# Kernel optimization log

Measured on AMD Instinct MI355X. Metric: run time of the kernel, lower is better.

The kernel has to match this reference:

```python
import jax, jax.numpy as jnp
import numpy as np

B, T, H, NH = 16, 2048, 1024, 16
HD = H // NH  # 64
IN0, IN1 = 256, 512  # modality input sizes needing projection; modality 2 is already H


def _ln(x, g, b, eps=1e-5):
    m = jnp.mean(x, axis=-1, keepdims=True)
    v = jnp.mean((x - m) ** 2, axis=-1, keepdims=True)
    return (x - m) / jnp.sqrt(v + eps) * g + b


def setup_inputs() -> dict:
    key = jax.random.key(0)
    ks = jax.random.split(key, 24)
    s = 0.02
    d = {
        'x0': jax.random.normal(ks[0], (B, T, IN0), jnp.float32),
        'x1': jax.random.normal(ks[1], (B, T, IN1), jnp.float32),
        'x2': jax.random.normal(ks[2], (B, T, H), jnp.float32),
        'static_context': jax.random.normal(ks[3], (B, T, H), jnp.float32),
        'Wp0': jax.random.normal(ks[4], (H, IN0), jnp.float32) * s,
        'bp0': jnp.zeros((H,), jnp.float32),
        'Wp1': jax.random.normal(ks[5], (H, IN1), jnp.float32) * s,
        'bp1': jnp.zeros((H,), jnp.float32),
        'Wq': jax.random.normal(ks[6], (H, H), jnp.float32) * s,
        'bq': jnp.zeros((H,), jnp.float32),
        'Wk': jax.random.normal(ks[7], (H, H), jnp.float32) * s,
        'bk': jnp.zeros((H,), jnp.float32),
        'Wv': jax.random.normal(ks[8], (H, H), jnp.float32) * s,
        'bv': jnp.zeros((H,), jnp.float32),
        'Wo': jax.random.normal(ks[9], (H, H), jnp.float32) * s,
        'bo': jnp.zeros((H,), jnp.float32),
        'query_token': jax.random.normal(ks[10], (H,), jnp.float32) * s,
        'g1': jnp.ones((H,), jnp.float32),
        'be1': jnp.zeros((H,), jnp.float32),
        'g2': jnp.ones((H,), jnp.float32),
        'be2': jnp.zeros((H,), jnp.float32),
        'W1': jax.random.normal(ks[11], (4 * H, H), jnp.float32) * s,
        'b1': jnp.zeros((4 * H,), jnp.float32),
        'W2': jax.random.normal(ks[12], (H, 4 * H), jnp.float32) * s,
        'b2': jnp.zeros((H,), jnp.float32),
    }
    return d


def _forward(x0, x1, x2, static_context, Wp0, bp0, Wp1, bp1, Wq, bq, Wk, bk, Wv, bv,
             Wo, bo, query_token, g1, be1, g2, be2, W1, b1, W2, b2):
    # project modalities to hidden size, stack -> [B, T, M, H]
    m0 = x0 @ Wp0.T + bp0
    m1 = x1 @ Wp1.T + bp1
    stacked = jnp.stack([m0, m1, x2], axis=2)  # [B,T,3,H]
    M = stacked.shape[2]
    # per-timestep single-query cross-attention over the M modality tokens,
    # batched over all B*T positions (equivalent to the torch per-t loop)
    q = query_token + static_context  # [B,T,H]
    Q = (q @ Wq.T + bq).reshape(B, T, NH, HD)
    K = (stacked @ Wk.T + bk).reshape(B, T, M, NH, HD)
    V = (stacked @ Wv.T + bv).reshape(B, T, M, NH, HD)
    scores = jnp.einsum('bthd,btmhd->bthm', Q, K) / jnp.sqrt(jnp.asarray(HD, Q.dtype))
    attn = jax.nn.softmax(scores, axis=-1)  # [B,T,NH,M]
    weights = attn.mean(axis=2)  # average over heads (torch default) -> [B,T,M]
    ctx = jnp.einsum('bthm,btmhd->bthd', attn, V).reshape(B, T, H)
    attn_out = ctx @ Wo.T + bo
    fused = _ln(attn_out, g1, be1)
    ff = jax.nn.gelu(fused @ W1.T + b1, approximate=False) @ W2.T + b2
    fused = _ln(fused + ff, g2, be2)
    return fused, weights


def reference(x0, x1, x2, static_context, Wp0, bp0, Wp1, bp1, Wq, bq, Wk, bk, Wv, bv,
              Wo, bo, query_token, g1, be1, g2, be2, W1, b1, W2, b2):
    return _forward(x0, x1, x2, static_context, Wp0, bp0, Wp1, bp1, Wq, bq, Wk, bk,
                    Wv, bv, Wo, bo, query_token, g1, be1, g2, be2, W1, b1, W2, b2)
```

## Files before the change

kernel.cpp:

```cpp
#include <hip/hip_runtime.h>
#include <hip/hip_bf16.h>
#include <math.h>

#define BT 32768
#define HH 1024

typedef unsigned short u16;
typedef __attribute__((ext_vector_type(4))) unsigned short u16x4;
typedef __attribute__((ext_vector_type(8))) __bf16 bf16x8;
typedef __attribute__((ext_vector_type(4))) float f32x4;

#define DEVI static __device__ __forceinline__

DEVI u16 f2bf(float f){
  unsigned u = __builtin_bit_cast(unsigned, f);
  u += 0x7FFFu + ((u >> 16) & 1u);
  return (u16)(u >> 16);
}
DEVI float bf2f(u16 h){
  unsigned u = ((unsigned)h) << 16;
  return __builtin_bit_cast(float, u);
}
DEVI void gl_lds16(const void* g, void* l){
  __builtin_amdgcn_global_load_lds((const __attribute__((address_space(1))) void*)g,
                                   (__attribute__((address_space(3))) void*)l, 16, 0, 0);
}
DEVI int swz(int row, int elem){ return elem ^ ((row & 7) << 3); }

__global__ void k_cast4(const float* __restrict__ s, u16* __restrict__ d, int n4){
  int i = blockIdx.x*blockDim.x + threadIdx.x;
  int st = gridDim.x*blockDim.x;
  for (; i < n4; i += st){
    float4 v = ((const float4*)s)[i];
    u16x4 o = { f2bf(v.x), f2bf(v.y), f2bf(v.z), f2bf(v.w) };
    ((u16x4*)d)[i] = o;
  }
}

__global__ void k_qb(const float* __restrict__ qt, const float* __restrict__ sc,
                     u16* __restrict__ d, int n4){
  int i = blockIdx.x*blockDim.x + threadIdx.x;
  int st = gridDim.x*blockDim.x;
  for (; i < n4; i += st){
    int e = i*4; int c = e & 1023;
    float4 v = *(const float4*)&sc[e];
    float4 q = *(const float4*)&qt[c];
    u16x4 o = { f2bf(v.x+q.x), f2bf(v.y+q.y), f2bf(v.z+q.z), f2bf(v.w+q.w) };
    ((u16x4*)d)[i] = o;
  }
}

__global__ void k_copyf(const float* __restrict__ s, float* __restrict__ d, int n){
  int i = blockIdx.x*blockDim.x + threadIdx.x;
  int st = gridDim.x*blockDim.x;
  for (; i < n; i += st) d[i] = s[i];
}

__global__ void k_transcast(const float* __restrict__ s, u16* __restrict__ d, int R, int C){
  __shared__ float tile[32][33];
  int c0 = blockIdx.x*32, r0 = blockIdx.y*32;
  int tx = threadIdx.x & 31, ty = threadIdx.x >> 5;
  #pragma unroll
  for (int i = 0; i < 32; i += 8) tile[ty+i][tx] = s[(size_t)(r0+ty+i)*C + c0+tx];
  __syncthreads();
  #pragma unroll
  for (int i = 0; i < 32; i += 8) d[(size_t)(c0+ty+i)*R + r0+tx] = f2bf(tile[tx][ty+i]);
}

__global__ void k_matvec(const u16* __restrict__ W, const float* __restrict__ x,
                         const float* __restrict__ badd, float* __restrict__ out, int K){
  int row = blockIdx.x*4 + (threadIdx.x>>6);
  int lane = threadIdx.x & 63;
  float s = 0.f;
  for (int k = lane; k < K; k += 64) s += bf2f(W[(size_t)row*K + k]) * x[k];
  #pragma unroll
  for (int m = 1; m < 64; m <<= 1) s += __shfl_xor(s, m);
  if (lane == 0) out[row] = s + badd[row];
}

__global__ __launch_bounds__(256, 3)
void k_gemm(const u16* __restrict__ A, int lda,
            const u16* __restrict__ B, int ldb, int K,
            const float* __restrict__ bias,
            u16* __restrict__ C, int ldc, int col0, int act)
{
  __shared__ u16 As[128*64];
  __shared__ u16 Bs[128*64];
  const int tid = threadIdx.x, lane = tid & 63, wid = tid >> 6;
  const int wr = wid >> 1, wc = wid & 1;
  const int r15 = lane & 15, g = lane >> 4;
  const int m0 = blockIdx.x * 128, n0 = blockIdx.y * 128;
  f32x4 acc[4][4] = {};

  for (int k0 = 0; k0 < K; k0 += 64){
    #pragma unroll
    for (int it = 0; it < 4; ++it){
      int c = it*256 + tid;
      int row = c >> 3;
      int ke = swz(row, (c & 7) * 8);
      gl_lds16(A + (size_t)(m0+row)*lda + (k0+ke), As + c*8);
      gl_lds16(B + (size_t)(n0+row)*ldb + (k0+ke), Bs + c*8);
    }
    __syncthreads();
    #pragma unroll
    for (int kk = 0; kk < 64; kk += 32){
      bf16x8 av[4], bvv[4];
      #pragma unroll
      for (int i = 0; i < 4; ++i){
        int row = wr*64 + i*16 + r15;
        av[i] = *(const bf16x8*)&As[row*64 + swz(row, kk + g*8)];
      }
      #pragma unroll
      for (int j = 0; j < 4; ++j){
        int row = wc*64 + j*16 + r15;
        bvv[j] = *(const bf16x8*)&Bs[row*64 + swz(row, kk + g*8)];
      }
      #pragma unroll
      for (int i = 0; i < 4; ++i)
        #pragma unroll
        for (int j = 0; j < 4; ++j)
          acc[i][j] = __builtin_amdgcn_mfma_f32_16x16x32_bf16(av[i], bvv[j], acc[i][j], 0, 0, 0);
    }
    __syncthreads();
  }
  #pragma unroll
  for (int j = 0; j < 4; ++j){
    int col = wc*64 + j*16 + r15;
    float bb = bias ? bias[n0 + col] : 0.f;
    #pragma unroll
    for (int i = 0; i < 4; ++i){
      #pragma unroll
      for (int jj = 0; jj < 4; ++jj){
        int row = wr*64 + i*16 + g*4 + jj;
        float v = acc[i][j][jj] + bb;
        if (act == 1) v = 0.5f * v * (1.f + erff(v * 0.70710678118654752f));
        C[(size_t)(m0+row)*ldc + col0 + n0 + col] = f2bf(v);
      }
    }
  }
}

__global__ __launch_bounds__(512, 4)
void k_attn2p(const u16* __restrict__ x0b, const u16* __restrict__ x1b, const u16* __restrict__ x2b,
              const u16* __restrict__ Wc0, const u16* __restrict__ Wc1, const u16* __restrict__ Wc2,
              const float* __restrict__ bc0, const float* __restrict__ bc1, const float* __restrict__ bc2,
              const u16* __restrict__ Qg, u16* __restrict__ ctx, float* __restrict__ wacc)
{
  __shared__ __align__(16) u16 As[128*64];
  __shared__ __align__(16) u16 Bs[128*64];
  __shared__ float Sl[2*128*3];

  const int tid = threadIdx.x, lane = tid & 63, wid = tid >> 6;
  const int wr = wid >> 1, h = wid & 1;
  const int r15 = lane & 15, g = lane >> 4;
  const int bid = blockIdx.x;
  const int bn = bid & 7, btb = bid >> 3;
  const int t0 = btb * 128, n0 = bn * 128;

  const u16* Xs[3] = { x0b, x1b, x2b };
  const u16* Ws[3] = { Wc0, Wc1, Wc2 };
  const float* Bc[3] = { bc0, bc1, bc2 };
  const int Ks[3] = { 256, 512, 1024 };

  const int srow = tid >> 3;
  const int scol = (tid & 7) * 8;

  #pragma unroll
  for (int m = 0; m < 3; ++m){
    const int K = Ks[m];
    const u16* X = Xs[m];
    const u16* W = Ws[m];
    f32x4 aK[2][4] = {};
    for (int k0 = 0; k0 < K; k0 += 64){
      #pragma unroll
      for (int l = 0; l < 2; ++l){
        int row = l*64 + srow;
        int ke = swz(row, scol);
        gl_lds16(X + (size_t)(t0+row)*K + k0 + ke, &As[row*64 + scol]);
        gl_lds16(W + (size_t)(n0+row)*K + k0 + ke, &Bs[row*64 + scol]);
      }
      __syncthreads();
      #pragma unroll
      for (int kk = 0; kk < 64; kk += 32){
        bf16x8 av[2], bv[4];
        #pragma unroll
        for (int i = 0; i < 2; ++i){
          int ra = wr*32 + i*16 + r15;
          av[i] = *(const bf16x8*)&As[ra*64 + swz(ra, kk + g*8)];
        }
        #pragma unroll
        for (int j = 0; j < 4; ++j){
          int rb = h*64 + j*16 + r15;
          bv[j] = *(const bf16x8*)&Bs[rb*64 + swz(rb, kk + g*8)];
        }
        #pragma unroll
        for (int i = 0; i < 2; ++i)
          #pragma unroll
          for (int j = 0; j < 4; ++j)
            aK[i][j] = __builtin_amdgcn_mfma_f32_16x16x32_bf16(av[i], bv[j], aK[i][j], 0, 0, 0);
      }
      __syncthreads();
    }
    float bkc[4];
    #pragma unroll
    for (int j = 0; j < 4; ++j) bkc[j] = Bc[m][n0 + h*64 + j*16 + r15];
    #pragma unroll
    for (int i = 0; i < 2; ++i){
      #pragma unroll
      for (int jj = 0; jj < 4; ++jj){
        int tt = wr*32 + i*16 + g*4 + jj;
        const u16* qrow = Qg + (size_t)(t0+tt)*1024 + n0 + h*64 + r15;
        float s = 0.f;
        #pragma unroll
        for (int j = 0; j < 4; ++j)
          s += (aK[i][j][jj] + bkc[j]) * bf2f(qrow[j*16]);
        s += __shfl_xor(s, 1); s += __shfl_xor(s, 2);
        s += __shfl_xor(s, 4); s += __shfl_xor(s, 8);
        if (r15 == 0) Sl[(h*128 + tt)*3 + m] = s * 0.125f;
      }
    }
  }
  __syncthreads();
  if (tid < 256){
    int h2 = tid >> 7, tt = tid & 127;
    int base = (h2*128 + tt)*3;
    float s0 = Sl[base+0], s1 = Sl[base+1], s2 = Sl[base+2];
    float mx = fmaxf(s0, fmaxf(s1, s2));
    float e0 = expf(s0-mx), e1 = expf(s1-mx), e2 = expf(s2-mx);
    float inv = 1.f/(e0+e1+e2);
    e0 *= inv; e1 *= inv; e2 *= inv;
    Sl[base+0] = e0; Sl[base+1] = e1; Sl[base+2] = e2;
    atomicAdd(&wacc[(size_t)(t0+tt)*3 + 0], e0*0.0625f);
    atomicAdd(&wacc[(size_t)(t0+tt)*3 + 1], e1*0.0625f);
    atomicAdd(&wacc[(size_t)(t0+tt)*3 + 2], e2*0.0625f);
  }
  __syncthreads();

  f32x4 ctxa[2][4] = {};
  #pragma unroll
  for (int m = 0; m < 3; ++m){
    const int K = Ks[m];
    const u16* X = Xs[m];
    const u16* W = Ws[m] + (size_t)1024*K;
    f32x4 aV[2][4] = {};
    for (int k0 = 0; k0 < K; k0 += 64){
      #pragma unroll
      for (int l = 0; l < 2; ++l){
        int row = l*64 + srow;
        int ke = swz(row, scol);
        gl_lds16(X + (size_t)(t0+row)*K + k0 + ke, &As[row*64 + scol]);
        gl_lds16(W + (size_t)(n0+row)*K + k0 + ke, &Bs[row*64 + scol]);
      }
      __syncthreads();
      #pragma unroll
      for (int kk = 0; kk < 64; kk += 32){
        bf16x8 av[2], bv[4];
        #pragma unroll
        for (int i = 0; i < 2; ++i){
          int ra = wr*32 + i*16 + r15;
          av[i] = *(const bf16x8*)&As[ra*64 + swz(ra, kk + g*8)];
        }
        #pragma unroll
        for (int j = 0; j < 4; ++j){
          int rb = h*64 + j*16 + r15;
          bv[j] = *(const bf16x8*)&Bs[rb*64 + swz(rb, kk + g*8)];
        }
        #pragma unroll
        for (int i = 0; i < 2; ++i)
          #pragma unroll
          for (int j = 0; j < 4; ++j)
            aV[i][j] = __builtin_amdgcn_mfma_f32_16x16x32_bf16(av[i], bv[j], aV[i][j], 0, 0, 0);
      }
      __syncthreads();
    }
    #pragma unroll
    for (int j = 0; j < 4; ++j){
      float bvv = Bc[m][1024 + n0 + h*64 + j*16 + r15];
      #pragma unroll
      for (int i = 0; i < 2; ++i){
        #pragma unroll
        for (int jj = 0; jj < 4; ++jj){
          int tt = wr*32 + i*16 + g*4 + jj;
          float p = Sl[(h*128 + tt)*3 + m];
          ctxa[i][j][jj] += p * (aV[i][j][jj] + bvv);
        }
      }
    }
  }
  #pragma unroll
  for (int i = 0; i < 2; ++i){
    #pragma unroll
    for (int jj = 0; jj < 4; ++jj){
      int tt = wr*32 + i*16 + g*4 + jj;
      #pragma unroll
      for (int j = 0; j < 4; ++j)
        ctx[(size_t)(t0+tt)*1024 + n0 + h*64 + j*16 + r15] = f2bf(ctxa[i][j][jj]);
    }
  }
}

__global__ __launch_bounds__(256)
void k_ln(const u16* __restrict__ X, const u16* __restrict__ R,
          const float* __restrict__ gam, const float* __restrict__ bet,
          u16* __restrict__ outb, float* __restrict__ outf)
{
  __shared__ float rs[4], rq[4];
  const int t = blockIdx.x, tid = threadIdx.x;
  const size_t base = (size_t)t*1024 + tid*4;
  u16x4 xv = *(const u16x4*)&X[base];
  float v[4];
  #pragma unroll
  for (int i = 0; i < 4; ++i) v[i] = bf2f(xv[i]);
  if (R){
    u16x4 rv = *(const u16x4*)&R[base];
    #pragma unroll
    for (int i = 0; i < 4; ++i) v[i] += bf2f(rv[i]);
  }
  float s = v[0]+v[1]+v[2]+v[3];
  float q = v[0]*v[0]+v[1]*v[1]+v[2]*v[2]+v[3]*v[3];
  #pragma unroll
  for (int m = 1; m < 64; m <<= 1){ s += __shfl_xor(s, m); q += __shfl_xor(q, m); }
  if ((tid & 63) == 0){ rs[tid>>6] = s; rq[tid>>6] = q; }
  __syncthreads();
  s = rs[0]+rs[1]+rs[2]+rs[3];
  q = rq[0]+rq[1]+rq[2]+rq[3];
  float mean = s * (1.f/1024.f);
  float var  = q * (1.f/1024.f) - mean*mean;
  float rstd = rsqrtf(var + 1e-5f);
  int c0 = tid*4;
  if (outb){
    u16x4 o;
    #pragma unroll
    for (int i = 0; i < 4; ++i) o[i] = f2bf((v[i]-mean)*rstd*gam[c0+i] + bet[c0+i]);
    *(u16x4*)&outb[base] = o;
  } else {
    float4 o;
    o.x = (v[0]-mean)*rstd*gam[c0+0] + bet[c0+0];
    o.y = (v[1]-mean)*rstd*gam[c0+1] + bet[c0+1];
    o.z = (v[2]-mean)*rstd*gam[c0+2] + bet[c0+2];
    o.w = (v[3]-mean)*rstd*gam[c0+3] + bet[c0+3];
    *(float4*)&outf[base] = o;
  }
}

extern "C" void kernel_launch(void* const* d_in, const int* in_sizes, int n_in,
                              void* d_out, int out_size, void* d_ws, size_t ws_size,
                              hipStream_t stream)
{
  (void)in_sizes; (void)n_in; (void)out_size;
  const float* x0  = (const float*)d_in[0];
  const float* x1  = (const float*)d_in[1];
  const float* x2  = (const float*)d_in[2];
  const float* sc  = (const float*)d_in[3];
  const float* Wp0 = (const float*)d_in[4];  const float* bp0 = (const float*)d_in[5];
  const float* Wp1 = (const float*)d_in[6];  const float* bp1 = (const float*)d_in[7];
  const float* Wq  = (const float*)d_in[8];  const float* bq  = (const float*)d_in[9];
  const float* Wk  = (const float*)d_in[10]; const float* bk  = (const float*)d_in[11];
  const float* Wv  = (const float*)d_in[12]; const float* bv  = (const float*)d_in[13];
  const float* Wo  = (const float*)d_in[14]; const float* bo  = (const float*)d_in[15];
  const float* qt  = (const float*)d_in[16];
  const float* g1  = (const float*)d_in[17]; const float* be1 = (const float*)d_in[18];
  const float* g2  = (const float*)d_in[19]; const float* be2 = (const float*)d_in[20];
  const float* W1  = (const float*)d_in[21]; const float* b1  = (const float*)d_in[22];
  const float* W2  = (const float*)d_in[23]; const float* b2  = (const float*)d_in[24];

  char* ws = (char*)d_ws;
  size_t off = 0;
  auto alloc = [&](size_t b)->char*{ char* p = ws + off; off += (b + 255) & ~(size_t)255; return p; };

  u16* Wqb   = (u16*)alloc((size_t)1024*1024*2);
  u16* Wob   = (u16*)alloc((size_t)1024*1024*2);
  u16* W1b   = (u16*)alloc((size_t)4096*1024*2);
  u16* W2b   = (u16*)alloc((size_t)1024*4096*2);
  u16* Wkvb  = (u16*)alloc((size_t)2048*1024*2);
  u16* Wp0t  = (u16*)alloc((size_t)256*1024*2);
  u16* Wp1t  = (u16*)alloc((size_t)512*1024*2);
  u16* Wkv0c = (u16*)alloc((size_t)2048*256*2);
  u16* Wkv1c = (u16*)alloc((size_t)2048*512*2);
  float* bc0 = (float*)alloc((size_t)2048*4);
  float* bc1 = (float*)alloc((size_t)2048*4);
  float* bc2 = (float*)alloc((size_t)2048*4);
  char* regX  = alloc((size_t)BT*(256+512+1024)*2);
  char* regQ1 = alloc((size_t)BT*1024*2);
  char* regQ2 = alloc((size_t)BT*1024*2);
  float* wacc = (float*)alloc((size_t)BT*3*4);
  if (off > ws_size) return;

  u16* x0b = (u16*)regX;
  u16* x1b = (u16*)(regX + (size_t)BT*256*2);
  u16* x2b = (u16*)(regX + (size_t)BT*768*2);
  u16* aob  = (u16*)regX;
  u16* ff2b = (u16*)regX;
  u16* qb   = (u16*)regQ1;
  u16* ctxb = (u16*)regQ1;
  u16* f1b  = (u16*)regQ1;
  u16* Qb   = (u16*)regQ2;
  u16* ff1c = (u16*)regQ2;

  hipMemsetAsync(wacc, 0, (size_t)BT*3*4, stream);

  dim3 B256(256), B512(512);
  auto cast4 = [&](const float* s, u16* d, int n, int grid){
    k_cast4<<<dim3(grid), B256, 0, stream>>>(s, d, n >> 2);
  };
  cast4(Wq, Wqb, 1024*1024, 1024);
  cast4(Wk, Wkvb, 1024*1024, 1024);
  cast4(Wv, Wkvb + (size_t)1024*1024, 1024*1024, 1024);
  cast4(Wo, Wob, 1024*1024, 1024);
  cast4(W1, W1b, 4096*1024, 1024);
  cast4(W2, W2b, 4096*1024, 1024);
  cast4(x0, x0b, BT*256, 1024);
  cast4(x1, x1b, BT*512, 1024);
  cast4(x2, x2b, BT*1024, 2048);
  k_transcast<<<dim3(8, 32),  B256, 0, stream>>>(Wp0, Wp0t, 1024, 256);
  k_transcast<<<dim3(16, 32), B256, 0, stream>>>(Wp1, Wp1t, 1024, 512);
  k_copyf<<<dim3(4), B256, 0, stream>>>(bk, bc2, 1024);
  k_copyf<<<dim3(4), B256, 0, stream>>>(bv, bc2 + 1024, 1024);
  k_matvec<<<dim3(512), B256, 0, stream>>>(Wkvb, bp0, bc2, bc0, 1024);
  k_matvec<<<dim3(512), B256, 0, stream>>>(Wkvb, bp1, bc2, bc1, 1024);
  k_qb<<<dim3(2048), B256, 0, stream>>>(qt, sc, qb, BT*256);

  k_gemm<<<dim3(16, 2), B256, 0, stream>>>(Wkvb, 1024, Wp0t, 1024, 1024, nullptr, Wkv0c, 256, 0, 0);
  k_gemm<<<dim3(16, 4), B256, 0, stream>>>(Wkvb, 1024, Wp1t, 1024, 1024, nullptr, Wkv1c, 512, 0, 0);

  k_gemm<<<dim3(BT/128, 8), B256, 0, stream>>>(qb, 1024, Wqb, 1024, 1024, bq, Qb, 1024, 0, 0);
  k_attn2p<<<dim3(BT/128*8), B512, 0, stream>>>(x0b, x1b, x2b, Wkv0c, Wkv1c, Wkvb,
                                                bc0, bc1, bc2, Qb, ctxb, wacc);
  k_gemm<<<dim3(BT/128, 8), B256, 0, stream>>>(ctxb, 1024, Wob, 1024, 1024, bo, aob, 1024, 0, 0);
  k_ln<<<dim3(BT), B256, 0, stream>>>(aob, nullptr, g1, be1, f1b, nullptr);

  for (int c = 0; c < 4; ++c){
    const u16* fa = f1b + (size_t)c*8192*1024;
    k_gemm<<<dim3(64, 32), B256, 0, stream>>>(fa, 1024, W1b, 1024, 1024, b1, ff1c, 4096, 0, 1);
    k_gemm<<<dim3(64, 8),  B256, 0, stream>>>(ff1c, 4096, W2b, 4096, 4096, b2,
                                              ff2b + (size_t)c*8192*1024, 1024, 0, 0);
  }
  float* outf = (float*)d_out;
  k_ln<<<dim3(BT), B256, 0, stream>>>(ff2b, f1b, g2, be2, nullptr, outf);
  k_copyf<<<dim3(384), B256, 0, stream>>>(wacc, outf + (size_t)BT*1024, BT*3);
}
```

Before: 1.591 ms.

## Add 256x256-tile pipelined GEMM with XCD-aware block mapping for large projections

Adds a new 512-thread GEMM kernel using 256x256 output tiles, double-buffered LDS with direct global-to-LDS loads interleaved with MFMA quarter-steps, and a block-id remap that groups tiles by XCD. It replaces the 128x128 GEMM for the Q, output and FFN projections, and remaps attention block indices for XCD locality. When workspace allows, the FFN runs in two larger chunks using a bigger intermediate buffer. The aim is more operand reuse per LDS load, better L2 locality and fewer launches, at the cost of higher register/LDS pressure and lower occupancy.

```diff
diff --git a/kernel.cpp b/kernel.cpp
--- a/kernel.cpp
+++ b/kernel.cpp
@@ -140,6 +140,119 @@
   }
 }
 
+__global__ __launch_bounds__(512, 2)
+void k_gemm8(const u16* __restrict__ A, int lda,
+             const u16* __restrict__ B, int ldb, int K,
+             const float* __restrict__ bias,
+             u16* __restrict__ C, int ldc, int act, int nn)
+{
+  __shared__ u16 As[2][2][128*64];
+  __shared__ u16 Bs[2][2][128*64];
+  const int tid = threadIdx.x, lane = tid & 63, wid = tid >> 6;
+  const int wr = wid >> 2, wc = wid & 3;
+  const int r15 = lane & 15, g = lane >> 4;
+  const int cpx = gridDim.x >> 3;
+  const int sid = ((int)blockIdx.x & 7) * cpx + ((int)blockIdx.x >> 3);
+  const int m0 = (sid / nn) * 256, n0 = (sid % nn) * 256;
+  const int nt = K >> 6;
+  f32x4 acc[8][4] = {};
+  const int srow = tid >> 3, scol = (tid & 7) * 8;
+
+  auto stA = [&](int buf, int half, int t){
+    int k0 = (t < nt ? t : nt-1) << 6;
+    #pragma unroll
+    for (int l = 0; l < 2; ++l){
+      int lr = l*64 + srow;
+      gl_lds16(A + (size_t)(m0 + half*128 + lr)*lda + k0 + swz(lr, scol),
+               &As[buf][half][lr*64 + scol]);
+    }
+  };
+  auto stB = [&](int buf, int half, int t){
+    int k0 = (t < nt ? t : nt-1) << 6;
+    #pragma unroll
+    for (int l = 0; l < 2; ++l){
+      int lr = l*64 + srow;
+      gl_lds16(B + (size_t)(n0 + half*128 + lr)*ldb + k0 + swz(lr, scol),
+               &Bs[buf][half][lr*64 + scol]);
+    }
+  };
+
+  bf16x8 av[4][2], bv[2][2];
+  auto loadq = [&](int buf, int MI, int NJ){
+    #pragma unroll
+    for (int i = 0; i < 4; ++i){
+      int r = wr*64 + i*16 + r15;
+      #pragma unroll
+      for (int k2 = 0; k2 < 2; ++k2)
+        av[i][k2] = *(const bf16x8*)&As[buf][MI][r*64 + swz(r, k2*32 + g*8)];
+    }
+    #pragma unroll
+    for (int j = 0; j < 2; ++j){
+      int cr = wc*32 + j*16 + r15;
+      #pragma unroll
+      for (int k2 = 0; k2 < 2; ++k2)
+        bv[j][k2] = *(const bf16x8*)&Bs[buf][NJ][cr*64 + swz(cr, k2*32 + g*8)];
+    }
+  };
+  auto mmaq = [&](int MI, int NJ){
+    __builtin_amdgcn_s_setprio(1);
+    #pragma unroll
+    for (int k2 = 0; k2 < 2; ++k2)
+      #pragma unroll
+      for (int i = 0; i < 4; ++i)
+        #pragma unroll
+        for (int j = 0; j < 2; ++j)
+          acc[MI*4+i][NJ*2+j] = __builtin_amdgcn_mfma_f32_16x16x32_bf16(
+              av[i][k2], bv[j][k2], acc[MI*4+i][NJ*2+j], 0, 0, 0);
+    __builtin_amdgcn_s_setprio(0);
+  };
+
+  stA(0,0,0); stA(0,1,0); stB(0,0,0); stB(0,1,0); stB(1,0,1); stA(1,0,1);
+  asm volatile("s_waitcnt vmcnt(4)" ::: "memory");
+  __builtin_amdgcn_s_barrier();
+
+  for (int t = 0; t < nt; ++t){
+    const int cur = t & 1, opp = cur ^ 1;
+    loadq(cur, 0, 0);
+    stA(opp, 1, t+1);
+    mmaq(0, 0);
+    asm volatile("s_waitcnt vmcnt(6) lgkmcnt(0)" ::: "memory");
+    __builtin_amdgcn_s_barrier();
+    loadq(cur, 1, 0);
+    stB(opp, 1, t+1);
+    mmaq(1, 0);
+    asm volatile("s_waitcnt lgkmcnt(0)" ::: "memory");
+    __builtin_amdgcn_s_barrier();
+    loadq(cur, 0, 1);
+    stB(cur, 0, t+2);
+    mmaq(0, 1);
+    asm volatile("s_waitcnt lgkmcnt(0)" ::: "memory");
+    __builtin_amdgcn_s_barrier();
+    loadq(cur, 1, 1);
+    stA(cur, 0, t+2);
+    mmaq(1, 1);
+    asm volatile("s_waitcnt vmcnt(6) lgkmcnt(0)" ::: "memory");
+    __builtin_amdgcn_s_barrier();
+  }
+  asm volatile("s_waitcnt vmcnt(0)" ::: "memory");
+
+  #pragma unroll
+  for (int jf = 0; jf < 4; ++jf){
+    int col = n0 + (jf>>1)*128 + wc*32 + (jf&1)*16 + r15;
+    float bb = bias ? bias[col] : 0.f;
+    #pragma unroll
+    for (int fi = 0; fi < 8; ++fi){
+      #pragma unroll
+      for (int jj = 0; jj < 4; ++jj){
+        int row = m0 + (fi>>2)*128 + wr*64 + (fi&3)*16 + g*4 + jj;
+        float v = acc[fi][jf][jj] + bb;
+        if (act == 1) v = 0.5f * v * (1.f + erff(v * 0.70710678118654752f));
+        C[(size_t)row*ldc + col] = f2bf(v);
+      }
+    }
+  }
+}
+
 __global__ __launch_bounds__(512, 4)
 void k_attn2p(const u16* __restrict__ x0b, const u16* __restrict__ x1b, const u16* __restrict__ x2b,
               const u16* __restrict__ Wc0, const u16* __restrict__ Wc1, const u16* __restrict__ Wc2,
@@ -154,7 +267,9 @@
   const int wr = wid >> 1, h = wid & 1;
   const int r15 = lane & 15, g = lane >> 4;
   const int bid = blockIdx.x;
-  const int bn = bid & 7, btb = bid >> 3;
+  const int xcd = bid & 7;
+  const int bn = (bid >> 3) & 7;
+  const int btb = (bid >> 6) * 8 + xcd;
   const int t0 = btb * 128, n0 = bn * 128;
 
   const u16* Xs[3] = { x0b, x1b, x2b };
@@ -385,6 +500,8 @@
   char* regQ2 = alloc((size_t)BT*1024*2);
   float* wacc = (float*)alloc((size_t)BT*3*4);
   if (off > ws_size) return;
+  u16* ff1big = nullptr;
+  if (off + (size_t)16384*4096*2 <= ws_size) ff1big = (u16*)alloc((size_t)16384*4096*2);
 
   u16* x0b = (u16*)regX;
   u16* x1b = (u16*)(regX + (size_t)BT*256*2);
@@ -395,7 +512,6 @@
   u16* ctxb = (u16*)regQ1;
   u16* f1b  = (u16*)regQ1;
   u16* Qb   = (u16*)regQ2;
-  u16* ff1c = (u16*)regQ2;
 
   hipMemsetAsync(wacc, 0, (size_t)BT*3*4, stream);
 
@@ -423,17 +539,27 @@
   k_gemm<<<dim3(16, 2), B256, 0, stream>>>(Wkvb, 1024, Wp0t, 1024, 1024, nullptr, Wkv0c, 256, 0, 0);
   k_gemm<<<dim3(16, 4), B256, 0, stream>>>(Wkvb, 1024, Wp1t, 1024, 1024, nullptr, Wkv1c, 512, 0, 0);
 
-  k_gemm<<<dim3(BT/128, 8), B256, 0, stream>>>(qb, 1024, Wqb, 1024, 1024, bq, Qb, 1024, 0, 0);
+  k_gemm8<<<dim3(512), B512, 0, stream>>>(qb, 1024, Wqb, 1024, 1024, bq, Qb, 1024, 0, 4);
   k_attn2p<<<dim3(BT/128*8), B512, 0, stream>>>(x0b, x1b, x2b, Wkv0c, Wkv1c, Wkvb,
                                                 bc0, bc1, bc2, Qb, ctxb, wacc);
-  k_gemm<<<dim3(BT/128, 8), B256, 0, stream>>>(ctxb, 1024, Wob, 1024, 1024, bo, aob, 1024, 0, 0);
+  k_gemm8<<<dim3(512), B512, 0, stream>>>(ctxb, 1024, Wob, 1024, 1024, bo, aob, 1024, 0, 4);
   k_ln<<<dim3(BT), B256, 0, stream>>>(aob, nullptr, g1, be1, f1b, nullptr);
 
-  for (int c = 0; c < 4; ++c){
-    const u16* fa = f1b + (size_t)c*8192*1024;
-    k_gemm<<<dim3(64, 32), B256, 0, stream>>>(fa, 1024, W1b, 1024, 1024, b1, ff1c, 4096, 0, 1);
-    k_gemm<<<dim3(64, 8),  B256, 0, stream>>>(ff1c, 4096, W2b, 4096, 4096, b2,
-                                              ff2b + (size_t)c*8192*1024, 1024, 0, 0);
+  if (ff1big){
+    for (int c = 0; c < 2; ++c){
+      const u16* fa = f1b + (size_t)c*16384*1024;
+      k_gemm8<<<dim3(1024), B512, 0, stream>>>(fa, 1024, W1b, 1024, 1024, b1, ff1big, 4096, 1, 16);
+      k_gemm8<<<dim3(256),  B512, 0, stream>>>(ff1big, 4096, W2b, 4096, 4096, b2,
+                                               ff2b + (size_t)c*16384*1024, 1024, 0, 4);
+    }
+  } else {
+    u16* ff1c = (u16*)regQ2;
+    for (int c = 0; c < 4; ++c){
+      const u16* fa = f1b + (size_t)c*8192*1024;
+      k_gemm8<<<dim3(512), B512, 0, stream>>>(fa, 1024, W1b, 1024, 1024, b1, ff1c, 4096, 1, 16);
+      k_gemm8<<<dim3(128), B512, 0, stream>>>(ff1c, 4096, W2b, 4096, 4096, b2,
+                                              ff2b + (size_t)c*8192*1024, 1024, 0, 4);
+    }
   }
   float* outf = (float*)d_out;
   k_ln<<<dim3(BT), B256, 0, stream>>>(ff2b, f1b, g2, be2, nullptr, outf);
```

After: 1.695 ms. 1.06x slower.

## Double-buffer attention K/V GEMM loop, remap blocks per XCD, replace atomics with partial buffer

Applied to the files above, without the earlier changes.

The fused attention kernel's K and V projection loops become one 28-step pipelined pass per projection. It uses double-buffered LDS and register prefetch of the next tile, with one barrier per step instead of two. This is meant to hide global load latency behind MFMA work. Block indices are remapped so blocks sharing the same time tile land on the same XCD, which should improve L2 reuse of the activations. Per-head atomic adds for the attention weights are replaced by writes into a partial buffer that a new kernel averages, which removes the atomics and the memset at the cost of a larger buffer.

```diff
diff --git a/kernel.cpp b/kernel.cpp
--- a/kernel.cpp
+++ b/kernel.cpp
@@ -7,6 +7,7 @@
 
 typedef unsigned short u16;
 typedef __attribute__((ext_vector_type(4))) unsigned short u16x4;
+typedef __attribute__((ext_vector_type(8))) unsigned short u16x8;
 typedef __attribute__((ext_vector_type(8))) __bf16 bf16x8;
 typedef __attribute__((ext_vector_type(4))) float f32x4;
 
@@ -54,6 +55,18 @@
   int i = blockIdx.x*blockDim.x + threadIdx.x;
   int st = gridDim.x*blockDim.x;
   for (; i < n; i += st) d[i] = s[i];
+}
+
+__global__ void k_wmean(const float* __restrict__ p, float* __restrict__ out, int n){
+  int i = blockIdx.x*blockDim.x + threadIdx.x;
+  int st = gridDim.x*blockDim.x;
+  for (; i < n; i += st){
+    int t = i/3, m = i - t*3;
+    float s = 0.f;
+    #pragma unroll
+    for (int h = 0; h < 16; ++h) s += p[(size_t)t*48 + h*3 + m];
+    out[i] = s * 0.0625f;
+  }
 }
 
 __global__ void k_transcast(const float* __restrict__ s, u16* __restrict__ d, int R, int C){
@@ -144,63 +157,104 @@
 void k_attn2p(const u16* __restrict__ x0b, const u16* __restrict__ x1b, const u16* __restrict__ x2b,
               const u16* __restrict__ Wc0, const u16* __restrict__ Wc1, const u16* __restrict__ Wc2,
               const float* __restrict__ bc0, const float* __restrict__ bc1, const float* __restrict__ bc2,
-              const u16* __restrict__ Qg, u16* __restrict__ ctx, float* __restrict__ wacc)
+              const u16* __restrict__ Qg, u16* __restrict__ ctx, float* __restrict__ pbuf)
 {
-  __shared__ __align__(16) u16 As[128*64];
-  __shared__ __align__(16) u16 Bs[128*64];
+  __shared__ __align__(16) u16 As[2][128*64];
+  __shared__ __align__(16) u16 Bs[2][128*64];
   __shared__ float Sl[2*128*3];
 
   const int tid = threadIdx.x, lane = tid & 63, wid = tid >> 6;
   const int wr = wid >> 1, h = wid & 1;
   const int r15 = lane & 15, g = lane >> 4;
   const int bid = blockIdx.x;
-  const int bn = bid & 7, btb = bid >> 3;
+  const int xcd = bid & 7, bn = (bid >> 3) & 7, btb = (bid >> 6) * 8 + xcd;
   const int t0 = btb * 128, n0 = bn * 128;
 
   const u16* Xs[3] = { x0b, x1b, x2b };
-  const u16* Ws[3] = { Wc0, Wc1, Wc2 };
   const float* Bc[3] = { bc0, bc1, bc2 };
   const int Ks[3] = { 256, 512, 1024 };
 
   const int srow = tid >> 3;
   const int scol = (tid & 7) * 8;
 
-  #pragma unroll
-  for (int m = 0; m < 3; ++m){
-    const int K = Ks[m];
-    const u16* X = Xs[m];
-    const u16* W = Ws[m];
-    f32x4 aK[2][4] = {};
-    for (int k0 = 0; k0 < K; k0 += 64){
+  auto smk = [&](int s, int& m, int& k0){
+    if (s < 4){ m = 0; k0 = s << 6; }
+    else if (s < 12){ m = 1; k0 = (s-4) << 6; }
+    else { m = 2; k0 = (s-12) << 6; }
+  };
+
+  auto run_pass = [&](const u16* W0, const u16* W1, const u16* W2, auto epi){
+    const u16* Wp[3] = { W0, W1, W2 };
+    f32x4 acc[2][4] = {};
+    u16x8 r0, r1, r2, r3;
+    auto pf = [&](int s){
+      int m, k0; smk(s, m, k0); int K = Ks[m];
+      const u16* X = Xs[m]; const u16* W = Wp[m];
+      r0 = *(const u16x8*)(X + (size_t)(t0+srow)*K + k0 + scol);
+      r1 = *(const u16x8*)(X + (size_t)(t0+64+srow)*K + k0 + scol);
+      r2 = *(const u16x8*)(W + (size_t)(n0+srow)*K + k0 + scol);
+      r3 = *(const u16x8*)(W + (size_t)(n0+64+srow)*K + k0 + scol);
+    };
+    auto stw = [&](int b){
+      *(u16x8*)&As[b][srow*64 + swz(srow, scol)] = r0;
+      *(u16x8*)&As[b][(64+srow)*64 + swz(64+srow, scol)] = r1;
+      *(u16x8*)&Bs[b][srow*64 + swz(srow, scol)] = r2;
+      *(u16x8*)&Bs[b][(64+srow)*64 + swz(64+srow, scol)] = r3;
+    };
+    {
+      int m, k0; smk(0, m, k0); int K = Ks[m];
+      const u16* X = Xs[m]; const u16* W = Wp[m];
       #pragma unroll
       for (int l = 0; l < 2; ++l){
         int row = l*64 + srow;
-        int ke = swz(row, scol);
-        gl_lds16(X + (size_t)(t0+row)*K + k0 + ke, &As[row*64 + scol]);
-        gl_lds16(W + (size_t)(n0+row)*K + k0 + ke, &Bs[row*64 + scol]);
-      }
-      __syncthreads();
-      #pragma unroll
-      for (int kk = 0; kk < 64; kk += 32){
-        bf16x8 av[2], bv[4];
+        gl_lds16(X + (size_t)(t0+row)*K + k0 + swz(row, scol), &As[0][row*64 + scol]);
+        gl_lds16(W + (size_t)(n0+row)*K + k0 + swz(row, scol), &Bs[0][row*64 + scol]);
+      }
+      asm volatile("s_waitcnt vmcnt(0)" ::: "memory");
+      pf(1);
+      __builtin_amdgcn_s_barrier();
+      __builtin_amdgcn_sched_barrier(0);
+    }
+    for (int s = 0; s < 28; ++s){
+      int m, k0; smk(s, m, k0);
+      const int buf = s & 1;
+      if (s < 27) stw(buf ^ 1);
+      if (s + 2 < 28) pf(s + 2);
+      #pragma unroll
+      for (int k2 = 0; k2 < 2; ++k2){
+        bf16x8 a2[2], b2[4];
         #pragma unroll
         for (int i = 0; i < 2; ++i){
           int ra = wr*32 + i*16 + r15;
-          av[i] = *(const bf16x8*)&As[ra*64 + swz(ra, kk + g*8)];
+          a2[i] = *(const bf16x8*)&As[buf][ra*64 + swz(ra, k2*32 + g*8)];
         }
         #pragma unroll
         for (int j = 0; j < 4; ++j){
           int rb = h*64 + j*16 + r15;
-          bv[j] = *(const bf16x8*)&Bs[rb*64 + swz(rb, kk + g*8)];
+          b2[j] = *(const bf16x8*)&Bs[buf][rb*64 + swz(rb, k2*32 + g*8)];
         }
         #pragma unroll
         for (int i = 0; i < 2; ++i)
           #pragma unroll
           for (int j = 0; j < 4; ++j)
-            aK[i][j] = __builtin_amdgcn_mfma_f32_16x16x32_bf16(av[i], bv[j], aK[i][j], 0, 0, 0);
-      }
-      __syncthreads();
-    }
+            acc[i][j] = __builtin_amdgcn_mfma_f32_16x16x32_bf16(a2[i], b2[j], acc[i][j], 0, 0, 0);
+      }
+      asm volatile("s_waitcnt lgkmcnt(0)" ::: "memory");
+      __builtin_amdgcn_s_barrier();
+      __builtin_amdgcn_sched_barrier(0);
+      int mn, kn; smk(s == 27 ? 27 : s+1, mn, kn);
+      if (s == 27 || mn != m){
+        epi(m, acc);
+        #pragma unroll
+        for (int i = 0; i < 2; ++i)
+          #pragma unroll
+          for (int j = 0; j < 4; ++j)
+            acc[i][j] = f32x4{0.f, 0.f, 0.f, 0.f};
+      }
+    }
+  };
+
+  run_pass(Wc0, Wc1, Wc2, [&](int m, f32x4 (&acc)[2][4]){
     float bkc[4];
     #pragma unroll
     for (int j = 0; j < 4; ++j) bkc[j] = Bc[m][n0 + h*64 + j*16 + r15];
@@ -210,17 +264,18 @@
       for (int jj = 0; jj < 4; ++jj){
         int tt = wr*32 + i*16 + g*4 + jj;
         const u16* qrow = Qg + (size_t)(t0+tt)*1024 + n0 + h*64 + r15;
-        float s = 0.f;
+        float sv = 0.f;
         #pragma unroll
         for (int j = 0; j < 4; ++j)
-          s += (aK[i][j][jj] + bkc[j]) * bf2f(qrow[j*16]);
-        s += __shfl_xor(s, 1); s += __shfl_xor(s, 2);
-        s += __shfl_xor(s, 4); s += __shfl_xor(s, 8);
-        if (r15 == 0) Sl[(h*128 + tt)*3 + m] = s * 0.125f;
-      }
-    }
-  }
+          sv += (acc[i][j][jj] + bkc[j]) * bf2f(qrow[j*16]);
+        sv += __shfl_xor(sv, 1); sv += __shfl_xor(sv, 2);
+        sv += __shfl_xor(sv, 4); sv += __shfl_xor(sv, 8);
+        if (r15 == 0) Sl[(h*128 + tt)*3 + m] = sv * 0.125f;
+      }
+    }
+  });
   __syncthreads();
+
   if (tid < 256){
     int h2 = tid >> 7, tt = tid & 127;
     int base = (h2*128 + tt)*3;
@@ -230,49 +285,14 @@
     float inv = 1.f/(e0+e1+e2);
     e0 *= inv; e1 *= inv; e2 *= inv;
     Sl[base+0] = e0; Sl[base+1] = e1; Sl[base+2] = e2;
-    atomicAdd(&wacc[(size_t)(t0+tt)*3 + 0], e0*0.0625f);
-    atomicAdd(&wacc[(size_t)(t0+tt)*3 + 1], e1*0.0625f);
-    atomicAdd(&wacc[(size_t)(t0+tt)*3 + 2], e2*0.0625f);
+    float* pp = pbuf + ((size_t)(t0+tt)*16 + (bn*2 + h2))*3;
+    pp[0] = e0; pp[1] = e1; pp[2] = e2;
   }
   __syncthreads();
 
   f32x4 ctxa[2][4] = {};
-  #pragma unroll
-  for (int m = 0; m < 3; ++m){
-    const int K = Ks[m];
-    const u16* X = Xs[m];
-    const u16* W = Ws[m] + (size_t)1024*K;
-    f32x4 aV[2][4] = {};
-    for (int k0 = 0; k0 < K; k0 += 64){
-      #pragma unroll
-      for (int l = 0; l < 2; ++l){
-        int row = l*64 + srow;
-        int ke = swz(row, scol);
-        gl_lds16(X + (size_t)(t0+row)*K + k0 + ke, &As[row*64 + scol]);
-        gl_lds16(W + (size_t)(n0+row)*K + k0 + ke, &Bs[row*64 + scol]);
-      }
-      __syncthreads();
-      #pragma unroll
-      for (int kk = 0; kk < 64; kk += 32){
-        bf16x8 av[2], bv[4];
-        #pragma unroll
-        for (int i = 0; i < 2; ++i){
-          int ra = wr*32 + i*16 + r15;
-          av[i] = *(const bf16x8*)&As[ra*64 + swz(ra, kk + g*8)];
-        }
-        #pragma unroll
-        for (int j = 0; j < 4; ++j){
-          int rb = h*64 + j*16 + r15;
-          bv[j] = *(const bf16x8*)&Bs[rb*64 + swz(rb, kk + g*8)];
-        }
-        #pragma unroll
-        for (int i = 0; i < 2; ++i)
-          #pragma unroll
-          for (int j = 0; j < 4; ++j)
-            aV[i][j] = __builtin_amdgcn_mfma_f32_16x16x32_bf16(av[i], bv[j], aV[i][j], 0, 0, 0);
-      }
-      __syncthreads();
-    }
+  run_pass(Wc0 + (size_t)1024*256, Wc1 + (size_t)1024*512, Wc2 + (size_t)1024*1024,
+           [&](int m, f32x4 (&acc)[2][4]){
     #pragma unroll
     for (int j = 0; j < 4; ++j){
       float bvv = Bc[m][1024 + n0 + h*64 + j*16 + r15];
@@ -282,11 +302,11 @@
         for (int jj = 0; jj < 4; ++jj){
           int tt = wr*32 + i*16 + g*4 + jj;
           float p = Sl[(h*128 + tt)*3 + m];
-          ctxa[i][j][jj] += p * (aV[i][j][jj] + bvv);
+          ctxa[i][j][jj] += p * (acc[i][j][jj] + bvv);
         }
       }
     }
-  }
+  });
   #pragma unroll
   for (int i = 0; i < 2; ++i){
     #pragma unroll
@@ -383,7 +403,7 @@
   char* regX  = alloc((size_t)BT*(256+512+1024)*2);
   char* regQ1 = alloc((size_t)BT*1024*2);
   char* regQ2 = alloc((size_t)BT*1024*2);
-  float* wacc = (float*)alloc((size_t)BT*3*4);
+  float* pbuf = (float*)alloc((size_t)BT*48*4);
   if (off > ws_size) return;
 
   u16* x0b = (u16*)regX;
@@ -396,8 +416,6 @@
   u16* f1b  = (u16*)regQ1;
   u16* Qb   = (u16*)regQ2;
   u16* ff1c = (u16*)regQ2;
-
-  hipMemsetAsync(wacc, 0, (size_t)BT*3*4, stream);
 
   dim3 B256(256), B512(512);
   auto cast4 = [&](const float* s, u16* d, int n, int grid){
@@ -425,7 +443,7 @@
 
   k_gemm<<<dim3(BT/128, 8), B256, 0, stream>>>(qb, 1024, Wqb, 1024, 1024, bq, Qb, 1024, 0, 0);
   k_attn2p<<<dim3(BT/128*8), B512, 0, stream>>>(x0b, x1b, x2b, Wkv0c, Wkv1c, Wkvb,
-                                                bc0, bc1, bc2, Qb, ctxb, wacc);
+                                                bc0, bc1, bc2, Qb, ctxb, pbuf);
   k_gemm<<<dim3(BT/128, 8), B256, 0, stream>>>(ctxb, 1024, Wob, 1024, 1024, bo, aob, 1024, 0, 0);
   k_ln<<<dim3(BT), B256, 0, stream>>>(aob, nullptr, g1, be1, f1b, nullptr);
 
@@ -437,5 +455,5 @@
   }
   float* outf = (float*)d_out;
   k_ln<<<dim3(BT), B256, 0, stream>>>(ff2b, f1b, g2, be2, nullptr, outf);
-  k_copyf<<<dim3(384), B256, 0, stream>>>(wacc, outf + (size_t)BT*1024, BT*3);
-}
+  k_wmean<<<dim3(384), B256, 0, stream>>>(pbuf, outf + (size_t)BT*1024, BT*3);
+}
```

Result: slower. 1.645 ms (+3.4%).

## Split attention kernel into score, softmax, and prob-weighted V GEMM passes

Applied to the files above, without the earlier changes.

Splits the fused attention kernel into three stages. A score pass writes per-head scores to a buffer, a small kernel applies softmax and writes the head-averaged weights straight to the output, and a second GEMM pass computes the context. In that second pass, X is pre-scaled by the per-row, per-head probability before the MFMA, so all three modalities accumulate into one tile and the V bias is folded in at the end. It also moves from 512-thread blocks with 128x64 per-wave-pair tiles to 256-thread blocks with 64x64 per-wave tiles, remaps block IDs for XCD locality, and removes the atomics and final copy. In exchange it adds two extra launches, round-trips scores and probabilities through global memory, rescales X in registers on every tile, and adds bf16 rounding to the scaled X.

```diff
diff --git a/kernel.cpp b/kernel.cpp
--- a/kernel.cpp
+++ b/kernel.cpp
@@ -7,6 +7,7 @@
 
 typedef unsigned short u16;
 typedef __attribute__((ext_vector_type(4))) unsigned short u16x4;
+typedef __attribute__((ext_vector_type(8))) unsigned short u16x8;
 typedef __attribute__((ext_vector_type(8))) __bf16 bf16x8;
 typedef __attribute__((ext_vector_type(4))) float f32x4;
 
@@ -54,6 +55,30 @@
   int i = blockIdx.x*blockDim.x + threadIdx.x;
   int st = gridDim.x*blockDim.x;
   for (; i < n; i += st) d[i] = s[i];
+}
+
+__global__ void k_psm(const float* __restrict__ s, float* __restrict__ p,
+                      float* __restrict__ wout, int T){
+  int t = blockIdx.x*blockDim.x + threadIdx.x;
+  int st = gridDim.x*blockDim.x;
+  for (; t < T; t += st){
+    float a0 = 0.f, a1 = 0.f, a2 = 0.f;
+    #pragma unroll
+    for (int h = 0; h < 16; ++h){
+      const float* b = s + (size_t)t*48 + h*3;
+      float s0 = b[0], s1 = b[1], s2 = b[2];
+      float mx = fmaxf(s0, fmaxf(s1, s2));
+      float e0 = __expf(s0-mx), e1 = __expf(s1-mx), e2 = __expf(s2-mx);
+      float inv = 1.f/(e0+e1+e2);
+      e0 *= inv; e1 *= inv; e2 *= inv;
+      float* q = p + (size_t)t*48 + h*3;
+      q[0] = e0; q[1] = e1; q[2] = e2;
+      a0 += e0; a1 += e1; a2 += e2;
+    }
+    wout[(size_t)t*3+0] = a0*0.0625f;
+    wout[(size_t)t*3+1] = a1*0.0625f;
+    wout[(size_t)t*3+2] = a2*0.0625f;
+  }
 }
 
 __global__ void k_transcast(const float* __restrict__ s, u16* __restrict__ d, int R, int C){
@@ -140,21 +165,19 @@
   }
 }
 
-__global__ __launch_bounds__(512, 4)
-void k_attn2p(const u16* __restrict__ x0b, const u16* __restrict__ x1b, const u16* __restrict__ x2b,
+__global__ __launch_bounds__(256, 3)
+void k_attnp1(const u16* __restrict__ x0b, const u16* __restrict__ x1b, const u16* __restrict__ x2b,
               const u16* __restrict__ Wc0, const u16* __restrict__ Wc1, const u16* __restrict__ Wc2,
               const float* __restrict__ bc0, const float* __restrict__ bc1, const float* __restrict__ bc2,
-              const u16* __restrict__ Qg, u16* __restrict__ ctx, float* __restrict__ wacc)
+              const u16* __restrict__ Qg, float* __restrict__ sbuf)
 {
-  __shared__ __align__(16) u16 As[128*64];
-  __shared__ __align__(16) u16 Bs[128*64];
-  __shared__ float Sl[2*128*3];
-
+  __shared__ u16 As[128*64];
+  __shared__ u16 Bs[128*64];
   const int tid = threadIdx.x, lane = tid & 63, wid = tid >> 6;
-  const int wr = wid >> 1, h = wid & 1;
+  const int wr = wid >> 1, wc = wid & 1;
   const int r15 = lane & 15, g = lane >> 4;
   const int bid = blockIdx.x;
-  const int bn = bid & 7, btb = bid >> 3;
+  const int xcd = bid & 7, bn = (bid >> 3) & 7, btb = (bid >> 6) * 8 + xcd;
   const int t0 = btb * 128, n0 = bn * 128;
 
   const u16* Xs[3] = { x0b, x1b, x2b };
@@ -162,139 +185,166 @@
   const float* Bc[3] = { bc0, bc1, bc2 };
   const int Ks[3] = { 256, 512, 1024 };
 
-  const int srow = tid >> 3;
-  const int scol = (tid & 7) * 8;
+  f32x4 acc[4][4] = {};
 
   #pragma unroll
   for (int m = 0; m < 3; ++m){
     const int K = Ks[m];
     const u16* X = Xs[m];
     const u16* W = Ws[m];
-    f32x4 aK[2][4] = {};
     for (int k0 = 0; k0 < K; k0 += 64){
       #pragma unroll
-      for (int l = 0; l < 2; ++l){
-        int row = l*64 + srow;
-        int ke = swz(row, scol);
-        gl_lds16(X + (size_t)(t0+row)*K + k0 + ke, &As[row*64 + scol]);
-        gl_lds16(W + (size_t)(n0+row)*K + k0 + ke, &Bs[row*64 + scol]);
+      for (int it = 0; it < 4; ++it){
+        int c = it*256 + tid;
+        int row = c >> 3;
+        int ke = swz(row, (c & 7) * 8);
+        gl_lds16(X + (size_t)(t0+row)*K + (k0+ke), As + c*8);
+        gl_lds16(W + (size_t)(n0+row)*K + (k0+ke), Bs + c*8);
       }
       __syncthreads();
       #pragma unroll
       for (int kk = 0; kk < 64; kk += 32){
-        bf16x8 av[2], bv[4];
-        #pragma unroll
-        for (int i = 0; i < 2; ++i){
-          int ra = wr*32 + i*16 + r15;
-          av[i] = *(const bf16x8*)&As[ra*64 + swz(ra, kk + g*8)];
+        bf16x8 av[4], bvv[4];
+        #pragma unroll
+        for (int i = 0; i < 4; ++i){
+          int row = wr*64 + i*16 + r15;
+          av[i] = *(const bf16x8*)&As[row*64 + swz(row, kk + g*8)];
         }
         #pragma unroll
         for (int j = 0; j < 4; ++j){
-          int rb = h*64 + j*16 + r15;
-          bv[j] = *(const bf16x8*)&Bs[rb*64 + swz(rb, kk + g*8)];
+          int row = wc*64 + j*16 + r15;
+          bvv[j] = *(const bf16x8*)&Bs[row*64 + swz(row, kk + g*8)];
         }
         #pragma unroll
-        for (int i = 0; i < 2; ++i)
+        for (int i = 0; i < 4; ++i)
           #pragma unroll
           for (int j = 0; j < 4; ++j)
-            aK[i][j] = __builtin_amdgcn_mfma_f32_16x16x32_bf16(av[i], bv[j], aK[i][j], 0, 0, 0);
+            acc[i][j] = __builtin_amdgcn_mfma_f32_16x16x32_bf16(av[i], bvv[j], acc[i][j], 0, 0, 0);
       }
       __syncthreads();
     }
     float bkc[4];
     #pragma unroll
-    for (int j = 0; j < 4; ++j) bkc[j] = Bc[m][n0 + h*64 + j*16 + r15];
-    #pragma unroll
-    for (int i = 0; i < 2; ++i){
+    for (int j = 0; j < 4; ++j) bkc[j] = Bc[m][n0 + wc*64 + j*16 + r15];
+    #pragma unroll
+    for (int i = 0; i < 4; ++i){
       #pragma unroll
       for (int jj = 0; jj < 4; ++jj){
-        int tt = wr*32 + i*16 + g*4 + jj;
-        const u16* qrow = Qg + (size_t)(t0+tt)*1024 + n0 + h*64 + r15;
-        float s = 0.f;
+        int row = wr*64 + i*16 + g*4 + jj;
+        const u16* qrow = Qg + (size_t)(t0+row)*1024 + n0 + wc*64 + r15;
+        float sv = 0.f;
         #pragma unroll
         for (int j = 0; j < 4; ++j)
-          s += (aK[i][j][jj] + bkc[j]) * bf2f(qrow[j*16]);
-        s += __shfl_xor(s, 1); s += __shfl_xor(s, 2);
-        s += __shfl_xor(s, 4); s += __shfl_xor(s, 8);
-        if (r15 == 0) Sl[(h*128 + tt)*3 + m] = s * 0.125f;
-      }
-    }
+          sv += (acc[i][j][jj] + bkc[j]) * bf2f(qrow[j*16]);
+        sv += __shfl_xor(sv, 1); sv += __shfl_xor(sv, 2);
+        sv += __shfl_xor(sv, 4); sv += __shfl_xor(sv, 8);
+        if (r15 == 0) sbuf[((size_t)(t0+row)*16 + bn*2 + wc)*3 + m] = sv * 0.125f;
+      }
+    }
+    #pragma unroll
+    for (int i = 0; i < 4; ++i)
+      #pragma unroll
+      for (int j = 0; j < 4; ++j)
+        acc[i][j] = f32x4{0.f, 0.f, 0.f, 0.f};
+  }
+}
+
+__global__ __launch_bounds__(256, 3)
+void k_attnp2(const u16* __restrict__ x0b, const u16* __restrict__ x1b, const u16* __restrict__ x2b,
+              const u16* __restrict__ Wc0, const u16* __restrict__ Wc1, const u16* __restrict__ Wc2,
+              const float* __restrict__ bc0, const float* __restrict__ bc1, const float* __restrict__ bc2,
+              const float* __restrict__ pbuf, u16* __restrict__ ctx)
+{
+  __shared__ u16 As[2][128*64];
+  __shared__ u16 Bs[128*64];
+  __shared__ float pl[768];
+  const int tid = threadIdx.x, lane = tid & 63, wid = tid >> 6;
+  const int wr = wid >> 1, wc = wid & 1;
+  const int r15 = lane & 15, g = lane >> 4;
+  const int bid = blockIdx.x;
+  const int xcd = bid & 7, bn = (bid >> 3) & 7, btb = (bid >> 6) * 8 + xcd;
+  const int t0 = btb * 128, n0 = bn * 128;
+
+  const u16* Xs[3] = { x0b, x1b, x2b };
+  const u16* Ws[3] = { Wc0, Wc1, Wc2 };
+  const float* Bc[3] = { bc0, bc1, bc2 };
+  const int Ks[3] = { 256, 512, 1024 };
+
+  for (int idx = tid; idx < 768; idx += 256){
+    int r = idx / 6, rem = idx - r*6;
+    int h = rem / 3, m = rem - h*3;
+    pl[idx] = pbuf[((size_t)(t0+r)*16 + bn*2 + h)*3 + m];
   }
   __syncthreads();
-  if (tid < 256){
-    int h2 = tid >> 7, tt = tid & 127;
-    int base = (h2*128 + tt)*3;
-    float s0 = Sl[base+0], s1 = Sl[base+1], s2 = Sl[base+2];
-    float mx = fmaxf(s0, fmaxf(s1, s2));
-    float e0 = expf(s0-mx), e1 = expf(s1-mx), e2 = expf(s2-mx);
-    float inv = 1.f/(e0+e1+e2);
-    e0 *= inv; e1 *= inv; e2 *= inv;
-    Sl[base+0] = e0; Sl[base+1] = e1; Sl[base+2] = e2;
-    atomicAdd(&wacc[(size_t)(t0+tt)*3 + 0], e0*0.0625f);
-    atomicAdd(&wacc[(size_t)(t0+tt)*3 + 1], e1*0.0625f);
-    atomicAdd(&wacc[(size_t)(t0+tt)*3 + 2], e2*0.0625f);
-  }
-  __syncthreads();
-
-  f32x4 ctxa[2][4] = {};
+
+  const int hh = tid >> 7, rr = tid & 127;
+  f32x4 acc[4][4] = {};
+
   #pragma unroll
   for (int m = 0; m < 3; ++m){
     const int K = Ks[m];
     const u16* X = Xs[m];
     const u16* W = Ws[m] + (size_t)1024*K;
-    f32x4 aV[2][4] = {};
+    const float psc = pl[rr*6 + hh*3 + m];
     for (int k0 = 0; k0 < K; k0 += 64){
-      #pragma unroll
-      for (int l = 0; l < 2; ++l){
-        int row = l*64 + srow;
-        int ke = swz(row, scol);
-        gl_lds16(X + (size_t)(t0+row)*K + k0 + ke, &As[row*64 + scol]);
-        gl_lds16(W + (size_t)(n0+row)*K + k0 + ke, &Bs[row*64 + scol]);
+      const u16* xrow = X + (size_t)(t0+rr)*K + k0;
+      #pragma unroll
+      for (int c0 = 0; c0 < 8; ++c0){
+        u16x8 v = *(const u16x8*)(xrow + c0*8);
+        u16x8 o;
+        #pragma unroll
+        for (int e = 0; e < 8; ++e) o[e] = f2bf(bf2f(v[e]) * psc);
+        *(u16x8*)&As[hh][rr*64 + swz(rr, c0*8)] = o;
+      }
+      #pragma unroll
+      for (int it = 0; it < 4; ++it){
+        int c = it*256 + tid;
+        int row = c >> 3;
+        int ke = swz(row, (c & 7) * 8);
+        gl_lds16(W + (size_t)(n0+row)*K + (k0+ke), Bs + c*8);
       }
       __syncthreads();
       #pragma unroll
       for (int kk = 0; kk < 64; kk += 32){
-        bf16x8 av[2], bv[4];
-        #pragma unroll
-        for (int i = 0; i < 2; ++i){
-          int ra = wr*32 + i*16 + r15;
-          av[i] = *(const bf16x8*)&As[ra*64 + swz(ra, kk + g*8)];
+        bf16x8 av[4], bvv[4];
+        #pragma unroll
+        for (int i = 0; i < 4; ++i){
+          int row = wr*64 + i*16 + r15;
+          av[i] = *(const bf16x8*)&As[wc][row*64 + swz(row, kk + g*8)];
         }
         #pragma unroll
         for (int j = 0; j < 4; ++j){
-          int rb = h*64 + j*16 + r15;
-          bv[j] = *(const bf16x8*)&Bs[rb*64 + swz(rb, kk + g*8)];
+          int row = wc*64 + j*16 + r15;
+          bvv[j] = *(const bf16x8*)&Bs[row*64 + swz(row, kk + g*8)];
         }
         #pragma unroll
-        for (int i = 0; i < 2; ++i)
+        for (int i = 0; i < 4; ++i)
           #pragma unroll
           for (int j = 0; j < 4; ++j)
-            aV[i][j] = __builtin_amdgcn_mfma_f32_16x16x32_bf16(av[i], bv[j], aV[i][j], 0, 0, 0);
+            acc[i][j] = __builtin_amdgcn_mfma_f32_16x16x32_bf16(av[i], bvv[j], acc[i][j], 0, 0, 0);
       }
       __syncthreads();
     }
-    #pragma unroll
-    for (int j = 0; j < 4; ++j){
-      float bvv = Bc[m][1024 + n0 + h*64 + j*16 + r15];
-      #pragma unroll
-      for (int i = 0; i < 2; ++i){
-        #pragma unroll
-        for (int jj = 0; jj < 4; ++jj){
-          int tt = wr*32 + i*16 + g*4 + jj;
-          float p = Sl[(h*128 + tt)*3 + m];
-          ctxa[i][j][jj] += p * (aV[i][j][jj] + bvv);
-        }
-      }
-    }
-  }
-  #pragma unroll
-  for (int i = 0; i < 2; ++i){
+  }
+  float bvc[3][4];
+  #pragma unroll
+  for (int m = 0; m < 3; ++m)
+    #pragma unroll
+    for (int j = 0; j < 4; ++j)
+      bvc[m][j] = Bc[m][1024 + n0 + wc*64 + j*16 + r15];
+  #pragma unroll
+  for (int i = 0; i < 4; ++i){
     #pragma unroll
     for (int jj = 0; jj < 4; ++jj){
-      int tt = wr*32 + i*16 + g*4 + jj;
-      #pragma unroll
-      for (int j = 0; j < 4; ++j)
-        ctx[(size_t)(t0+tt)*1024 + n0 + h*64 + j*16 + r15] = f2bf(ctxa[i][j][jj]);
+      int row = wr*64 + i*16 + g*4 + jj;
+      float p0 = pl[row*6 + wc*3 + 0];
+      float p1 = pl[row*6 + wc*3 + 1];
+      float p2 = pl[row*6 + wc*3 + 2];
+      #pragma unroll
+      for (int j = 0; j < 4; ++j){
+        float v = acc[i][j][jj] + p0*bvc[0][j] + p1*bvc[1][j] + p2*bvc[2][j];
+        ctx[(size_t)(t0+row)*1024 + n0 + wc*64 + j*16 + r15] = f2bf(v);
+      }
     }
   }
 }
@@ -383,7 +433,8 @@
   char* regX  = alloc((size_t)BT*(256+512+1024)*2);
   char* regQ1 = alloc((size_t)BT*1024*2);
   char* regQ2 = alloc((size_t)BT*1024*2);
-  float* wacc = (float*)alloc((size_t)BT*3*4);
+  float* sbuf = (float*)alloc((size_t)BT*48*4);
+  float* pbuf = (float*)alloc((size_t)BT*48*4);
   if (off > ws_size) return;
 
   u16* x0b = (u16*)regX;
@@ -397,9 +448,7 @@
   u16* Qb   = (u16*)regQ2;
   u16* ff1c = (u16*)regQ2;
 
-  hipMemsetAsync(wacc, 0, (size_t)BT*3*4, stream);
-
-  dim3 B256(256), B512(512);
+  dim3 B256(256);
   auto cast4 = [&](const float* s, u16* d, int n, int grid){
     k_cast4<<<dim3(grid), B256, 0, stream>>>(s, d, n >> 2);
   };
@@ -424,8 +473,11 @@
   k_gemm<<<dim3(16, 4), B256, 0, stream>>>(Wkvb, 1024, Wp1t, 1024, 1024, nullptr, Wkv1c, 512, 0, 0);
 
   k_gemm<<<dim3(BT/128, 8), B256, 0, stream>>>(qb, 1024, Wqb, 1024, 1024, bq, Qb, 1024, 0, 0);
-  k_attn2p<<<dim3(BT/128*8), B512, 0, stream>>>(x0b, x1b, x2b, Wkv0c, Wkv1c, Wkvb,
-                                                bc0, bc1, bc2, Qb, ctxb, wacc);
+  k_attnp1<<<dim3(BT/128*8), B256, 0, stream>>>(x0b, x1b, x2b, Wkv0c, Wkv1c, Wkvb,
+                                                bc0, bc1, bc2, Qb, sbuf);
+  k_psm<<<dim3(128), B256, 0, stream>>>(sbuf, pbuf, (float*)d_out + (size_t)BT*1024, BT);
+  k_attnp2<<<dim3(BT/128*8), B256, 0, stream>>>(x0b, x1b, x2b, Wkv0c, Wkv1c, Wkvb,
+                                                bc0, bc1, bc2, pbuf, ctxb);
   k_gemm<<<dim3(BT/128, 8), B256, 0, stream>>>(ctxb, 1024, Wob, 1024, 1024, bo, aob, 1024, 0, 0);
   k_ln<<<dim3(BT), B256, 0, stream>>>(aob, nullptr, g1, be1, f1b, nullptr);
 
@@ -437,5 +489,4 @@
   }
   float* outf = (float*)d_out;
   k_ln<<<dim3(BT), B256, 0, stream>>>(ff2b, f1b, g2, be2, nullptr, outf);
-  k_copyf<<<dim3(384), B256, 0, stream>>>(wacc, outf + (size_t)BT*1024, BT*3);
-}
+}
```

New measurement: 1.710 ms. 7.4% more time.
